# Kernel optimization log

Hardware: AMD Instinct MI355X
Metric: run time of the kernel (lower is better)

The kernel has to match this reference:

```python
import jax, jax.numpy as jnp
import numpy as np

KSIZE = 5
PAD = 2  # replicate padding per side for 'same' 5x5x5 box filter


def setup_inputs() -> dict:
    key = jax.random.key(0)
    # mp: [N, C, D, H, W] nonnegative probability maps
    mp = jax.random.uniform(key, (1, 21, 16, 256, 256), dtype=jnp.float32)
    return {"mp": mp}


def reference(mp):
    N, C, D, H, W = mp.shape
    # replicate ('edge') padding on D, H, W, then depthwise 5x5x5 box filter
    x = jnp.pad(mp, ((0, 0), (0, 0), (PAD, PAD), (PAD, PAD), (PAD, PAD)), mode="edge")
    k = jnp.full((C, 1, KSIZE, KSIZE, KSIZE), 1.0 / (KSIZE ** 3), dtype=mp.dtype)
    y = jax.lax.conv_general_dilated(
        x, k,
        window_strides=(1, 1, 1),
        padding="VALID",
        dimension_numbers=("NCDHW", "OIDHW", "NCDHW"),
        feature_group_count=C,
    )  # [N, C, D, H, W]

    # normalize over channel axis (torch permutes to put channels first; we keep axis=1)
    y = y / jnp.sum(y, axis=1, keepdims=True)

    # weighted-median selection: running cumulative sum over channels
    s = jnp.cumsum(y, axis=1)                     # [N, C, D, H, W]
    idx = jnp.arange(C).reshape(1, C, 1, 1, 1)    # channel indices

    # med0: LAST channel i with y[i] > 0 and cumsum < 0.5 (torch loop overwrites), default 0
    med0 = jnp.maximum(
        jnp.max(jnp.where((y > 0) & (s < 0.5), idx, -1), axis=1, keepdims=True), 0
    )
    # med1: torch sets med[1] only while med[1]==0, so the result is the FIRST
    # NONZERO channel with cumsum > 0.5 (i=0 qualifying leaves med[1]==0 and gets
    # overwritten by the next qualifying i); 0 if no nonzero channel qualifies.
    med1 = jnp.argmax((s > 0.5) & (idx > 0), axis=1, keepdims=True)

    keep = (idx == med0) | (idx == med1)
    return jnp.where(keep, y, jnp.zeros((), dtype=y.dtype))
```

## Files before the change

kernel.cpp:

```cpp
#include <hip/hip_runtime.h>

#define CC   21
#define DD   16
#define HH   256
#define WW   256
#define HWP  (HH * WW)
#define DHW  (DD * HWP)

typedef float f4a __attribute__((ext_vector_type(4), aligned(16)));
__device__ __forceinline__ f4a f4add(f4a a, f4a b) { return a + b; }

#define AROW 36
#define PYN  12
#define A_SZ (DD * PYN * AROW)

__global__ __launch_bounds__(256, 5) void dh_blur_kernel(const float* __restrict__ mp,
                                                         float* __restrict__ out) {
    __shared__ float A[A_SZ];

    const int w0 = blockIdx.x * 32;
    const int h0 = blockIdx.y * 8;
    const int ch = blockIdx.z;
    const int tid = threadIdx.x;
    const float* __restrict__ src = mp + (size_t)ch * DHW;

    if (tid < 192) {
        const int s   = (tid >= 96) ? 1 : 0;
        const int col = tid - s * 96;
        const int py  = col >> 3;
        const int x4  = col & 7;
        const int h   = min(HH - 1, max(0, h0 + py - 2));
        const float* colp = src + (size_t)h * WW + w0 + x4 * 4;

        f4a l[12];
#pragma unroll
        for (int m = 0; m < 12; ++m) {
            int dz = s * 8 + m;
            int d  = min(DD - 1, max(0, dz - 2));
            l[m] = *(const f4a*)(colp + (size_t)d * HWP);
        }
        f4a sum = f4add(f4add(f4add(l[0], l[1]), f4add(l[2], l[3])), l[4]);
#pragma unroll
        for (int i = 0; i < 8; ++i) {
            *(f4a*)(&A[((s * 8 + i) * PYN + py) * AROW + x4 * 4]) = sum;
            if (i < 7) sum = sum - l[i] + l[i + 5];
        }
    }
    __syncthreads();

#pragma unroll
    for (int it = 0; it < 4; ++it) {
        const int t    = tid + it * 256;
        const int x4   = t & 7;
        const int y    = (t >> 3) & 7;
        const int dout = t >> 6;

        const float* b = &A[(dout * PYN + y) * AROW + x4 * 4];
        f4a a = *(const f4a*)b;
#pragma unroll
        for (int k = 1; k < 5; ++k) a = f4add(a, *(const f4a*)(b + k * AROW));

        *(f4a*)(out + (size_t)ch * DHW + (size_t)dout * HWP
                + (h0 + y) * WW + w0 + x4 * 4) = a;
    }
}

#define ROWP 264

__global__ __launch_bounds__(256) void wmedian_kernel(float* __restrict__ y4) {
    __shared__ float R[CC * ROWP];

    const int h = blockIdx.x;
    const int d = blockIdx.y;
    const int tid = threadIdx.x;
    float* __restrict__ base = y4 + (size_t)d * HWP + (size_t)h * WW;

    for (int idx = tid; idx < CC * 64; idx += 256) {
        const int c  = idx >> 6;
        const int w4 = idx & 63;
        *(f4a*)(&R[c * ROWP + 4 + w4 * 4]) = *(const f4a*)(base + (size_t)c * DHW + w4 * 4);
    }
    if (tid < CC) {
        const float v0 = base[(size_t)tid * DHW];
        const float vL = base[(size_t)tid * DHW + (WW - 1)];
        R[tid * ROWP + 2]   = v0;
        R[tid * ROWP + 3]   = v0;
        R[tid * ROWP + 260] = vL;
        R[tid * ROWP + 261] = vL;
    }
    __syncthreads();

    const int w = tid;
    float v[CC];
    float tot = 0.f;
#pragma unroll
    for (int c = 0; c < CC; ++c) {
        const float* r = &R[c * ROWP + 2 + w];
        v[c] = ((((r[0] + r[1]) + r[2]) + r[3]) + r[4]);
        tot += v[c];
    }
    const float inv = 1.0f / tot;

    float s = 0.f, sv0 = 0.f, sv1 = 0.f;
    int m0 = 0, m1 = 0;
#pragma unroll
    for (int c = 0; c < CC; ++c) {
        const float yn = v[c] * inv;
        const float sn = s + yn;
        if (c == 0) { sv0 = yn; sv1 = yn; }
        if (v[c] > 0.f && sn < 0.5f) { m0 = c; sv0 = yn; }
        if (m1 == 0 && c > 0 && sn > 0.5f) { m1 = c; sv1 = yn; }
        s = sn;
    }

#pragma unroll
    for (int c = 0; c < CC; ++c) {
        base[(size_t)c * DHW + w] = (c == m0) ? sv0 : ((c == m1) ? sv1 : 0.f);
    }
}

extern "C" void kernel_launch(void* const* d_in, const int* in_sizes, int n_in,
                              void* d_out, int out_size, void* d_ws, size_t ws_size,
                              hipStream_t stream) {
    const float* mp = (const float*)d_in[0];
    float* out = (float*)d_out;

    dh_blur_kernel<<<dim3(WW / 32, HH / 8, CC), 256, 0, stream>>>(mp, out);
    wmedian_kernel<<<dim3(HH, DD), 256, 0, stream>>>(out);
}
```

Baseline: 194.9 us.

## Fuse 3D box blur and weighted-median selection into one kernel

Replaces the two-kernel pipeline (D/H blur written to the output, then a W-blur plus median pass that rereads it) with one kernel. Each block now holds all 21 channels for a small 2x32 spatial tile over 8 depth slices, does the D and H sums in registers, keeps them in shared memory, and finishes the W sum, normalization and median selection there. This removes the intermediate global write and reread. In exchange the halo overhead is larger (6 rows read for 2 output rows, extra columns), only 128 threads do the second phase, and occupancy drops because of the larger shared-memory footprint.

```diff
diff --git a/kernel.cpp b/kernel.cpp
--- a/kernel.cpp
+++ b/kernel.cpp
@@ -10,112 +10,119 @@
 typedef float f4a __attribute__((ext_vector_type(4), aligned(16)));
 __device__ __forceinline__ f4a f4add(f4a a, f4a b) { return a + b; }
 
-#define AROW 36
-#define PYN  12
-#define A_SZ (DD * PYN * AROW)
+#define CH_STRIDE (8 * 2 * 36)
+#define A_SZ      (CC * CH_STRIDE)
 
-__global__ __launch_bounds__(256, 5) void dh_blur_kernel(const float* __restrict__ mp,
-                                                         float* __restrict__ out) {
+__global__ __launch_bounds__(256, 3) void fused_kernel(const float* __restrict__ mp,
+                                                       float* __restrict__ out) {
     __shared__ float A[A_SZ];
+    const int tid = threadIdx.x;
 
-    const int w0 = blockIdx.x * 32;
-    const int h0 = blockIdx.y * 8;
-    const int ch = blockIdx.z;
-    const int tid = threadIdx.x;
-    const float* __restrict__ src = mp + (size_t)ch * DHW;
+    const int idx = blockIdx.x;
+    const int o   = idx >> 3;
+    const int ht  = (idx & 7) * 16 + (o & 15);
+    const int wt  = (o >> 4) & 7;
+    const int s   = o >> 7;
+    const int w0  = wt * 32;
+    const int h0  = ht * 2;
 
-    if (tid < 192) {
-        const int s   = (tid >= 96) ? 1 : 0;
-        const int col = tid - s * 96;
-        const int py  = col >> 3;
-        const int x4  = col & 7;
-        const int h   = min(HH - 1, max(0, h0 + py - 2));
-        const float* colp = src + (size_t)h * WW + w0 + x4 * 4;
+    if (tid < 189) {
+        const int ch  = tid / 9;
+        const int jjq = tid - ch * 9;
+        int lw = w0 - 2 + jjq * 4;
+        const bool lo = (lw < 0);
+        const bool hi = (lw > WW - 4);
+        lw = lo ? 0 : (hi ? (WW - 4) : lw);
+        const float* __restrict__ src = mp + (size_t)ch * DHW + lw;
 
-        f4a l[12];
+        f4a ha[8], hb[8];
 #pragma unroll
-        for (int m = 0; m < 12; ++m) {
-            int dz = s * 8 + m;
-            int d  = min(DD - 1, max(0, dz - 2));
-            l[m] = *(const f4a*)(colp + (size_t)d * HWP);
+        for (int r = 0; r < 6; ++r) {
+            const int hh = min(HH - 1, max(0, h0 + r - 2));
+            const float* rowp = src + (size_t)hh * WW;
+            f4a l[12];
+#pragma unroll
+            for (int m = 0; m < 12; ++m) {
+                const int dz = s * 8 + m;
+                const int d  = min(DD - 1, max(0, dz - 2));
+                l[m] = *(const f4a*)(rowp + (size_t)d * HWP);
+            }
+            f4a sum = f4add(f4add(f4add(l[0], l[1]), f4add(l[2], l[3])), l[4]);
+#pragma unroll
+            for (int i = 0; i < 8; ++i) {
+                if (r == 0)      ha[i] = sum;
+                else if (r < 5)  ha[i] = f4add(ha[i], sum);
+                if (r == 1)      hb[i] = sum;
+                else if (r > 1)  hb[i] = f4add(hb[i], sum);
+                if (i < 7) sum = sum - l[i] + l[i + 5];
+            }
         }
-        f4a sum = f4add(f4add(f4add(l[0], l[1]), f4add(l[2], l[3])), l[4]);
 #pragma unroll
         for (int i = 0; i < 8; ++i) {
-            *(f4a*)(&A[((s * 8 + i) * PYN + py) * AROW + x4 * 4]) = sum;
-            if (i < 7) sum = sum - l[i] + l[i + 5];
+            f4a oa = ha[i], ob = hb[i];
+            if (lo) { oa = f4a{oa.x, oa.x, oa.x, oa.y}; ob = f4a{ob.x, ob.x, ob.x, ob.y}; }
+            if (hi) { oa = f4a{oa.z, oa.w, oa.w, oa.w}; ob = f4a{ob.z, ob.w, ob.w, ob.w}; }
+            float* ap = &A[ch * CH_STRIDE + i * 72 + jjq * 4];
+            *(f4a*)(ap)      = oa;
+            *(f4a*)(ap + 36) = ob;
         }
     }
     __syncthreads();
 
+    if (tid < 128) {
+        const int wq = tid & 7;
+        const int h  = (tid >> 3) & 1;
+        const int d  = tid >> 4;
+        const float* __restrict__ base = &A[d * 72 + h * 36 + wq * 4];
+
+        float tot[4] = {0.f, 0.f, 0.f, 0.f};
 #pragma unroll
-    for (int it = 0; it < 4; ++it) {
-        const int t    = tid + it * 256;
-        const int x4   = t & 7;
-        const int y    = (t >> 3) & 7;
-        const int dout = t >> 6;
+        for (int c = 0; c < CC; ++c) {
+            const f4a a0 = *(const f4a*)(base + c * CH_STRIDE);
+            const f4a a1 = *(const f4a*)(base + c * CH_STRIDE + 4);
+            tot[0] += ((((a0.x + a0.y) + a0.z) + a0.w) + a1.x);
+            tot[1] += ((((a0.y + a0.z) + a0.w) + a1.x) + a1.y);
+            tot[2] += ((((a0.z + a0.w) + a1.x) + a1.y) + a1.z);
+            tot[3] += ((((a0.w + a1.x) + a1.y) + a1.z) + a1.w);
+        }
+        float inv[4];
+#pragma unroll
+        for (int p = 0; p < 4; ++p) inv[p] = 1.0f / tot[p];
 
-        const float* b = &A[(dout * PYN + y) * AROW + x4 * 4];
-        f4a a = *(const f4a*)b;
+        float sa[4] = {0.f, 0.f, 0.f, 0.f};
+        float v0[4], v1[4];
+        int m0[4] = {0, 0, 0, 0}, m1[4] = {0, 0, 0, 0};
 #pragma unroll
-        for (int k = 1; k < 5; ++k) a = f4add(a, *(const f4a*)(b + k * AROW));
+        for (int c = 0; c < CC; ++c) {
+            const f4a a0 = *(const f4a*)(base + c * CH_STRIDE);
+            const f4a a1 = *(const f4a*)(base + c * CH_STRIDE + 4);
+            float v[4];
+            v[0] = ((((a0.x + a0.y) + a0.z) + a0.w) + a1.x);
+            v[1] = ((((a0.y + a0.z) + a0.w) + a1.x) + a1.y);
+            v[2] = ((((a0.z + a0.w) + a1.x) + a1.y) + a1.z);
+            v[3] = ((((a0.w + a1.x) + a1.y) + a1.z) + a1.w);
+#pragma unroll
+            for (int p = 0; p < 4; ++p) {
+                const float yn = v[p] * inv[p];
+                const float sn = sa[p] + yn;
+                if (c == 0) { v0[p] = yn; v1[p] = yn; }
+                if (v[p] > 0.f && sn < 0.5f) { m0[p] = c; v0[p] = yn; }
+                if (m1[p] == 0 && c > 0 && sn > 0.5f) { m1[p] = c; v1[p] = yn; }
+                sa[p] = sn;
+            }
+        }
 
-        *(f4a*)(out + (size_t)ch * DHW + (size_t)dout * HWP
-                + (h0 + y) * WW + w0 + x4 * 4) = a;
-    }
-}
-
-#define ROWP 264
-
-__global__ __launch_bounds__(256) void wmedian_kernel(float* __restrict__ y4) {
-    __shared__ float R[CC * ROWP];
-
-    const int h = blockIdx.x;
-    const int d = blockIdx.y;
-    const int tid = threadIdx.x;
-    float* __restrict__ base = y4 + (size_t)d * HWP + (size_t)h * WW;
-
-    for (int idx = tid; idx < CC * 64; idx += 256) {
-        const int c  = idx >> 6;
-        const int w4 = idx & 63;
-        *(f4a*)(&R[c * ROWP + 4 + w4 * 4]) = *(const f4a*)(base + (size_t)c * DHW + w4 * 4);
-    }
-    if (tid < CC) {
-        const float v0 = base[(size_t)tid * DHW];
-        const float vL = base[(size_t)tid * DHW + (WW - 1)];
-        R[tid * ROWP + 2]   = v0;
-        R[tid * ROWP + 3]   = v0;
-        R[tid * ROWP + 260] = vL;
-        R[tid * ROWP + 261] = vL;
-    }
-    __syncthreads();
-
-    const int w = tid;
-    float v[CC];
-    float tot = 0.f;
+        float* __restrict__ dst = out + (size_t)(s * 8 + d) * HWP
+                                + (size_t)(h0 + h) * WW + w0 + wq * 4;
 #pragma unroll
-    for (int c = 0; c < CC; ++c) {
-        const float* r = &R[c * ROWP + 2 + w];
-        v[c] = ((((r[0] + r[1]) + r[2]) + r[3]) + r[4]);
-        tot += v[c];
-    }
-    const float inv = 1.0f / tot;
-
-    float s = 0.f, sv0 = 0.f, sv1 = 0.f;
-    int m0 = 0, m1 = 0;
-#pragma unroll
-    for (int c = 0; c < CC; ++c) {
-        const float yn = v[c] * inv;
-        const float sn = s + yn;
-        if (c == 0) { sv0 = yn; sv1 = yn; }
-        if (v[c] > 0.f && sn < 0.5f) { m0 = c; sv0 = yn; }
-        if (m1 == 0 && c > 0 && sn > 0.5f) { m1 = c; sv1 = yn; }
-        s = sn;
-    }
-
-#pragma unroll
-    for (int c = 0; c < CC; ++c) {
-        base[(size_t)c * DHW + w] = (c == m0) ? sv0 : ((c == m1) ? sv1 : 0.f);
+        for (int c = 0; c < CC; ++c) {
+            f4a ov;
+            ov.x = (c == m0[0]) ? v0[0] : ((c == m1[0]) ? v1[0] : 0.f);
+            ov.y = (c == m0[1]) ? v0[1] : ((c == m1[1]) ? v1[1] : 0.f);
+            ov.z = (c == m0[2]) ? v0[2] : ((c == m1[2]) ? v1[2] : 0.f);
+            ov.w = (c == m0[3]) ? v0[3] : ((c == m1[3]) ? v1[3] : 0.f);
+            *(f4a*)(dst + (size_t)c * DHW) = ov;
+        }
     }
 }
 
@@ -125,6 +132,5 @@
     const float* mp = (const float*)d_in[0];
     float* out = (float*)d_out;
 
-    dh_blur_kernel<<<dim3(WW / 32, HH / 8, CC), 256, 0, stream>>>(mp, out);
-    wmedian_kernel<<<dim3(HH, DD), 256, 0, stream>>>(out);
+    fused_kernel<<<2048, 256, 0, stream>>>(mp, out);
 }
```

Measured after the change: 205.1 us. 5.2% more time.
